# Kernel tuning notes

Hardware: AMD Instinct MI355X
Metric: run time of the kernel (lower is better)

Reference implementation:

```python
import jax, jax.numpy as jnp
import numpy as np

N, F, OUT = 8192, 256, 256


def setup_inputs() -> dict:
    key = jax.random.key(0)
    ks = jax.random.split(key, 8)
    s = 1.0 / np.sqrt(F)
    return {
        "features": jax.random.normal(ks[0], (N, F), jnp.float32),
        "key_features": jax.random.normal(ks[1], (N, F), jnp.float32),
        "adj_matrix": jax.random.uniform(ks[2], (N, N), jnp.float32),
        "W_d": jax.random.normal(ks[3], (2 * F, F), jnp.float32) * (1.0 / np.sqrt(2 * F)),
        "b_d": jnp.zeros((F,), jnp.float32),
        "W_o": jax.random.normal(ks[4], (F, OUT), jnp.float32) * s,
        "b_o": jnp.zeros((OUT,), jnp.float32),
        "W_a": jax.random.normal(ks[5], (F, F), jnp.float32) * s,
        "b_a": jnp.zeros((F,), jnp.float32),
        "W_ao": jax.random.normal(ks[6], (F, OUT), jnp.float32) * s,
        "b_ao": jnp.zeros((OUT,), jnp.float32),
    }


def reference(features, key_features, adj_matrix, W_d, b_d, W_o, b_o, W_a, b_a, W_ao, b_ao):
    n = features.shape[0]
    # masked softmax over rows; self-loop (diagonal) masked out
    neg = jnp.asarray(-1e9, adj_matrix.dtype)
    logits = adj_matrix * 5.0 + jnp.eye(n, dtype=adj_matrix.dtype) * neg
    a = jax.nn.softmax(logits, axis=-1)  # [N, N]
    # sum_j a_ij * concat(x_i, x_j) == concat(x_i * rowsum_i, (A @ X)_i)
    rowsum = jnp.sum(a, axis=-1, keepdims=True)  # == 1, kept for faithfulness
    agg = a @ features  # [N, F]
    neigh = jnp.concatenate([features * rowsum, agg], axis=-1)  # [N, 2F]
    neigh_distill = neigh @ W_d + b_d
    feature_updated = jnp.tanh((features - neigh_distill) @ W_o + b_o)
    # aggregate branch (withAgg=True)
    key_agg = (a @ key_features) @ W_a + b_a
    feature_aggregate = jnp.tanh((key_features + key_agg) @ W_ao + b_ao)
    return (feature_updated, feature_aggregate)
```

## Files before the change

kernel.cpp:

```cpp
#include <hip/hip_runtime.h>
#include <stdint.h>
#include <math.h>


typedef __attribute__((ext_vector_type(4)))  short bf16x4_t;
typedef __attribute__((ext_vector_type(8)))  short bf16x8_t;
typedef __attribute__((ext_vector_type(4)))  float f32x4_t;
typedef __attribute__((ext_vector_type(16))) float f32x16_t;

#define MFMA32(A, B, C) __builtin_amdgcn_mfma_f32_32x32x16_bf16(A, B, C, 0, 0, 0)
#define MFMA16(A, B, C) __builtin_amdgcn_mfma_f32_16x16x32_bf16(A, B, C, 0, 0, 0)

__device__ __forceinline__ unsigned short f2bf(float x) {
    union { float f; unsigned u; } c; c.f = x;
    unsigned u = c.u;
    return (unsigned short)((u + 0x7fffu + ((u >> 16) & 1u)) >> 16);
}
__device__ __forceinline__ unsigned pack2bf(float a, float b) {
    return (unsigned)f2bf(a) | ((unsigned)f2bf(b) << 16);
}
__device__ __forceinline__ float bflo(unsigned u) {
    union { unsigned u; float f; } c; c.u = u << 16; return c.f;
}
__device__ __forceinline__ float bfhi(unsigned u) {
    union { unsigned u; float f; } c; c.u = u & 0xffff0000u; return c.f;
}

__global__ __launch_bounds__(256) void transpose_f32_bf16(
    const float* __restrict__ src, unsigned short* __restrict__ dst, int R, int C)
{
    __shared__ float tile[32][33];
    const int x  = threadIdx.x & 31;
    const int y4 = (threadIdx.x >> 5) * 4;
    const int r0 = blockIdx.x * 32;
    const int c0 = blockIdx.y * 32;
#pragma unroll
    for (int i = 0; i < 4; ++i)
        tile[y4 + i][x] = src[(size_t)(r0 + y4 + i) * C + c0 + x];
    __syncthreads();
#pragma unroll
    for (int i = 0; i < 4; ++i)
        dst[(size_t)(c0 + y4 + i) * R + r0 + x] = f2bf(tile[x][y4 + i]);
}

__global__ __launch_bounds__(256) void pack_half(
    const float* __restrict__ src, unsigned* __restrict__ dst)
{
    const int idx = blockIdx.x * 256 + threadIdx.x;
    const int row = idx >> 7, cp = idx & 127;
    float2 v = *(const float2*)(src + (size_t)row * 256 + cp * 2);
    dst[(size_t)row * 256 + cp] = pack2bf(v.x, v.y);
}

__global__ __launch_bounds__(256) void compose1(
    const float* __restrict__ W_d, const float* __restrict__ W_o,
    unsigned short* __restrict__ W1t)
{
    __shared__ float wrow[256];
    const int k = blockIdx.x, t = threadIdx.x;
    wrow[t] = W_d[(size_t)k * 256 + t];
    __syncthreads();
    float acc = 0.f;
#pragma unroll 8
    for (int m = 0; m < 256; ++m) acc = fmaf(wrow[m], W_o[(size_t)m * 256 + t], acc);
    const float v = (k < 256 ? W_o[(size_t)k * 256 + t] : 0.f) - acc;
    W1t[(size_t)t * 512 + k] = f2bf(v);
}

__global__ __launch_bounds__(256) void compose2(
    const float* __restrict__ W_a, const float* __restrict__ W_ao,
    unsigned short* __restrict__ W2t)
{
    __shared__ float wrow[256];
    const int k = blockIdx.x, t = threadIdx.x;
    float v;
    if (k < 256) {
        v = W_ao[(size_t)k * 256 + t];
    } else {
        wrow[t] = W_a[(size_t)(k - 256) * 256 + t];
        __syncthreads();
        float acc = 0.f;
#pragma unroll 8
        for (int m = 0; m < 256; ++m) acc = fmaf(wrow[m], W_ao[(size_t)m * 256 + t], acc);
        v = acc;
    }
    W2t[(size_t)t * 512 + k] = f2bf(v);
}

__global__ __launch_bounds__(256) void biasC(
    const float* __restrict__ b_d, const float* __restrict__ b_o,
    const float* __restrict__ b_a, const float* __restrict__ b_ao,
    const float* __restrict__ W_o, const float* __restrict__ W_ao,
    float* __restrict__ c1, float* __restrict__ c2)
{
    const int t = threadIdx.x;
    float a1 = 0.f, a2 = 0.f;
#pragma unroll 8
    for (int m = 0; m < 256; ++m) {
        a1 = fmaf(b_d[m], W_o [(size_t)m * 256 + t], a1);
        a2 = fmaf(b_a[m], W_ao[(size_t)m * 256 + t], a2);
    }
    c1[t] = b_o[t] - a1;
    c2[t] = b_ao[t] + a2;
}

#define ROWS 128
#define KSLICE 2048
#define NIT 64
#define NCH 16
#define ASTRIDE 36

__global__ __launch_bounds__(1024) void exp_gemm(
    const float* __restrict__ adj, const unsigned short* __restrict__ Xt,
    unsigned short* __restrict__ Upart, float* __restrict__ sSp)
{
    __shared__ unsigned short sA[2][4][ROWS * ASTRIDE];

    const int t = threadIdx.x;
    const int w = t >> 6, lane = t & 63, q = lane >> 5, l31 = lane & 31;
    const int rb = blockIdx.x >> 2, h = blockIdx.x & 3;
    const int row0 = rb * ROWS, kbase = h * KSLICE;

    const int srow = t >> 3, skoff = (t & 7) * 4;
    const int sgrow = row0 + srow;
    const float* adj_row = adj + (size_t)sgrow * 8192 + kbase + skoff;
    const int swoff = srow * ASTRIDE + skoff;

    const unsigned short* bptr = Xt + (size_t)(w * 32 + l31) * 8192 + kbase + q * 8;

    float rs = 0.f;
    f32x16_t acc[4];
#pragma unroll
    for (int mt = 0; mt < 4; ++mt)
#pragma unroll
        for (int e = 0; e < 16; ++e) acc[mt][e] = 0.f;

    bf16x8_t bq[4][2];
    float4 qaA[4], qaB[4];

    auto stageChunk = [&](int cidx, const float4 (&qa)[4], int buf) {
        unsigned short* sb = &sA[buf][0][0] + swoff;
#pragma unroll
        for (int ks = 0; ks < 4; ++ks) {
            const float4 v = qa[ks];
            float e0 = __expf(5.f * v.x);
            float e1 = __expf(5.f * v.y);
            float e2 = __expf(5.f * v.z);
            float e3 = __expf(5.f * v.w);
            const int gk = kbase + (cidx * 4 + ks) * 32 + skoff;
            if (gk + 0 == sgrow) e0 = 0.f;
            if (gk + 1 == sgrow) e1 = 0.f;
            if (gk + 2 == sgrow) e2 = 0.f;
            if (gk + 3 == sgrow) e3 = 0.f;
            rs += (e0 + e1) + (e2 + e3);
            uint2 p; p.x = pack2bf(e0, e1); p.y = pack2bf(e2, e3);
            *(uint2*)(sb + ks * (ROWS * ASTRIDE)) = p;
        }
    };

    auto phase = [&](int c, float4 (&qaPre)[4], const float4 (&qaStg)[4], int buf) {
        if (c + 2 < NCH) {
#pragma unroll
            for (int ks = 0; ks < 4; ++ks)
                qaPre[ks] = *(const float4*)(adj_row + (size_t)((c + 2) * 4 + ks) * 32);
        }
        if (c + 1 < NCH) stageChunk(c + 1, qaStg, buf ^ 1);
#pragma unroll
        for (int u = 0; u < 4; ++u) {
            const int j = c * 4 + u;
            int jn = j + 2; if (jn >= NIT) jn = 0;
            bq[(u + 2) & 3][0] = *(const bf16x8_t*)(bptr + (size_t)jn * 32);
            bq[(u + 2) & 3][1] = *(const bf16x8_t*)(bptr + (size_t)jn * 32 + 16);
            const unsigned short* sa = &sA[buf][u][0] + l31 * ASTRIDE + q * 8;
#pragma unroll
            for (int s = 0; s < 2; ++s)
#pragma unroll
                for (int mt = 0; mt < 4; ++mt) {
                    const unsigned short* p = sa + mt * (32 * ASTRIDE) + s * 16;
                    bf16x4_t lo = *(const bf16x4_t*)p;
                    bf16x4_t hi = *(const bf16x4_t*)(p + 4);
                    bf16x8_t a = __builtin_shufflevector(lo, hi, 0, 1, 2, 3, 4, 5, 6, 7);
                    acc[mt] = MFMA32(a, bq[u][s], acc[mt]);
                }
        }
        asm volatile("s_waitcnt lgkmcnt(0)\n\ts_barrier" ::: "memory");
    };

#pragma unroll
    for (int ks = 0; ks < 4; ++ks)
        qaA[ks] = *(const float4*)(adj_row + (size_t)ks * 32);
#pragma unroll
    for (int ks = 0; ks < 4; ++ks)
        qaB[ks] = *(const float4*)(adj_row + (size_t)(4 + ks) * 32);
    stageChunk(0, qaA, 0);
    bq[0][0] = *(const bf16x8_t*)(bptr + 0);
    bq[0][1] = *(const bf16x8_t*)(bptr + 16);
    bq[1][0] = *(const bf16x8_t*)(bptr + 32);
    bq[1][1] = *(const bf16x8_t*)(bptr + 48);
    asm volatile("s_waitcnt lgkmcnt(0)\n\ts_barrier" ::: "memory");

    for (int c0 = 0; c0 < NCH; c0 += 2) {
        phase(c0,     qaA, qaB, 0);
        phase(c0 + 1, qaB, qaA, 1);
    }

    rs += __shfl_xor(rs, 1);
    rs += __shfl_xor(rs, 2);
    rs += __shfl_xor(rs, 4);
    if ((t & 7) == 0) sSp[h * 8192 + sgrow] = rs;

    unsigned short* up = Upart + (size_t)h * (8192 * 512) + (size_t)row0 * 512 + (w * 32 + l31);
#pragma unroll
    for (int mt = 0; mt < 4; ++mt)
#pragma unroll
        for (int reg = 0; reg < 16; ++reg) {
            const int lrow = mt * 32 + (reg & 3) + 8 * (reg >> 2) + 4 * q;
            up[(size_t)lrow * 512] = f2bf(acc[mt][reg]);
        }
}

__global__ __launch_bounds__(256) void finalize_agg(
    const unsigned* __restrict__ Upart, const float* __restrict__ sSp,
    unsigned* __restrict__ XcatN, unsigned* __restrict__ Kcat)
{
    const int row = blockIdx.x, t = threadIdx.x;
    const float inv = 1.f / (sSp[row] + sSp[8192 + row] + sSp[16384 + row] + sSp[24576 + row]);
    const unsigned* u = Upart + (size_t)row * 256 + t;
    float lo = 0.f, hi = 0.f;
#pragma unroll
    for (int hh = 0; hh < 4; ++hh) {
        const unsigned v = u[(size_t)hh * (8192 * 256)];
        lo += bflo(v); hi += bfhi(v);
    }
    const unsigned res = pack2bf(lo * inv, hi * inv);
    if (t < 128) XcatN[(size_t)row * 256 + 128 + t] = res;
    else         Kcat [(size_t)row * 256 + t];
    if (t >= 128) Kcat[(size_t)row * 256 + t] = res;
}

__global__ __launch_bounds__(256) void gemm_out(
    const unsigned short* __restrict__ A, const unsigned short* __restrict__ Wt,
    const float* __restrict__ cvec, float* __restrict__ out)
{
    __shared__ unsigned short sAm[32 * ASTRIDE];
    __shared__ unsigned short sB[256 * ASTRIDE];
    __shared__ float sBias[256];

    const int t = threadIdx.x, w = t >> 6, lane = t & 63;
    const int m_lo = lane & 15, quad = lane >> 4;
    const int row0 = blockIdx.x * 32;
    sBias[t] = cvec[t];

    f32x4_t acc[2][4];
#pragma unroll
    for (int a = 0; a < 2; ++a)
#pragma unroll
        for (int b = 0; b < 4; ++b)
#pragma unroll
            for (int e = 0; e < 4; ++e) acc[a][b][e] = 0.f;

    for (int ks = 0; ks < 16; ++ks) {
        const int k0 = ks * 32;
        __syncthreads();
        if (t < 128) {
            bf16x8_t v = *(const bf16x8_t*)(A + (size_t)(row0 + (t >> 2)) * 512 + k0 + (t & 3) * 8);
            unsigned short* d = &sAm[(t >> 2) * ASTRIDE + (t & 3) * 8];
            *(bf16x4_t*)d       = __builtin_shufflevector(v, v, 0, 1, 2, 3);
            *(bf16x4_t*)(d + 4) = __builtin_shufflevector(v, v, 4, 5, 6, 7);
        }
        {
            const unsigned short* src = Wt + (size_t)t * 512 + k0;
            unsigned short* d = &sB[t * ASTRIDE];
#pragma unroll
            for (int j = 0; j < 4; ++j) {
                bf16x8_t v = *(const bf16x8_t*)(src + j * 8);
                *(bf16x4_t*)(d + j * 8)     = __builtin_shufflevector(v, v, 0, 1, 2, 3);
                *(bf16x4_t*)(d + j * 8 + 4) = __builtin_shufflevector(v, v, 4, 5, 6, 7);
            }
        }
        __syncthreads();
        bf16x8_t a0, a1;
        {
            const unsigned short* p = &sAm[m_lo * ASTRIDE + quad * 8];
            bf16x4_t lo = *(const bf16x4_t*)p, hi = *(const bf16x4_t*)(p + 4);
            a0 = __builtin_shufflevector(lo, hi, 0, 1, 2, 3, 4, 5, 6, 7);
            p += 16 * ASTRIDE;
            lo = *(const bf16x4_t*)p; hi = *(const bf16x4_t*)(p + 4);
            a1 = __builtin_shufflevector(lo, hi, 0, 1, 2, 3, 4, 5, 6, 7);
        }
#pragma unroll
        for (int nt = 0; nt < 4; ++nt) {
            const unsigned short* p = &sB[(w * 64 + nt * 16 + m_lo) * ASTRIDE + quad * 8];
            bf16x4_t lo = *(const bf16x4_t*)p, hi = *(const bf16x4_t*)(p + 4);
            bf16x8_t b = __builtin_shufflevector(lo, hi, 0, 1, 2, 3, 4, 5, 6, 7);
            acc[0][nt] = MFMA16(a0, b, acc[0][nt]);
            acc[1][nt] = MFMA16(a1, b, acc[1][nt]);
        }
    }

#pragma unroll
    for (int mt = 0; mt < 2; ++mt)
#pragma unroll
        for (int nt = 0; nt < 4; ++nt) {
            const int col = w * 64 + nt * 16 + m_lo;
#pragma unroll
            for (int r = 0; r < 4; ++r) {
                const int row = row0 + mt * 16 + quad * 4 + r;
                out[(size_t)row * 256 + col] = tanhf(acc[mt][nt][r] + sBias[col]);
            }
        }
}

extern "C" void kernel_launch(void* const* d_in, const int* in_sizes, int n_in,
                              void* d_out, int out_size, void* d_ws, size_t ws_size,
                              hipStream_t stream) {
    const float* features = (const float*)d_in[0];
    const float* key      = (const float*)d_in[1];
    const float* adj      = (const float*)d_in[2];
    const float* W_d  = (const float*)d_in[3];
    const float* b_d  = (const float*)d_in[4];
    const float* W_o  = (const float*)d_in[5];
    const float* b_o  = (const float*)d_in[6];
    const float* W_a  = (const float*)d_in[7];
    const float* b_a  = (const float*)d_in[8];
    const float* W_ao = (const float*)d_in[9];
    const float* b_ao = (const float*)d_in[10];

    float* out1 = (float*)d_out;
    float* out2 = out1 + (size_t)8192 * 256;

    char* ws = (char*)d_ws;
    unsigned short* XcatN = (unsigned short*)(ws);
    unsigned short* Kcat  = (unsigned short*)(ws +  8388608);
    unsigned short* Xt    = (unsigned short*)(ws + 16777216);
    unsigned short* Upart = (unsigned short*)(ws + 25165824);
    float*          sSp   = (float*)         (ws + 58720256);
    unsigned short* W1t   = (unsigned short*)(ws + 58851328);
    unsigned short* W2t   = (unsigned short*)(ws + 59113472);
    float*          c1    = (float*)         (ws + 59375616);
    float*          c2    = (float*)         (ws + 59376640);

    dim3 blk(256);
    transpose_f32_bf16<<<dim3(256, 8), blk, 0, stream>>>(features, Xt, 8192, 256);
    transpose_f32_bf16<<<dim3(256, 8), blk, 0, stream>>>(key, Xt + (size_t)256 * 8192, 8192, 256);
    pack_half<<<4096, blk, 0, stream>>>(features, (unsigned*)XcatN);
    pack_half<<<4096, blk, 0, stream>>>(key, (unsigned*)Kcat);
    compose1<<<512, blk, 0, stream>>>(W_d, W_o, W1t);
    compose2<<<512, blk, 0, stream>>>(W_a, W_ao, W2t);
    biasC<<<1, blk, 0, stream>>>(b_d, b_o, b_a, b_ao, W_o, W_ao, c1, c2);

    exp_gemm<<<256, dim3(1024), 0, stream>>>(adj, Xt, Upart, sSp);
    finalize_agg<<<8192, blk, 0, stream>>>((const unsigned*)Upart, sSp,
                                           (unsigned*)XcatN, (unsigned*)Kcat);

    gemm_out<<<256, blk, 0, stream>>>(XcatN, W1t, c1, out1);
    gemm_out<<<256, blk, 0, stream>>>(Kcat,  W2t, c2, out2);
}
```

Measured before the change: 590.3 us.

## Restructure exp_gemm with async global-to-LDS loads and split output columns

The exp-weighted aggregation GEMM now streams adj tiles straight into LDS with global_load_lds, using a three-slot raw buffer. A separate pass applies exp and the diagonal mask and converts to a double-buffered bf16 tile. The grid is doubled to 512 blocks of 512 threads, each covering half of the 512 output columns, which is meant to raise occupancy and overlap memory with MFMA. The cost is that each adj tile is loaded and exponentiated by two blocks, doubling that traffic and exp work unless L2 absorbs the repeat loads. A dead load in finalize_agg is also removed.

New measurement: 607.0 us. 1.03x slower.

```diff
diff --git a/kernel.cpp b/kernel.cpp
--- a/kernel.cpp
+++ b/kernel.cpp
@@ -24,6 +24,12 @@
 }
 __device__ __forceinline__ float bfhi(unsigned u) {
     union { unsigned u; float f; } c; c.u = u & 0xffff0000u; return c.f;
+}
+
+__device__ __forceinline__ void dma16(const float* g, float* lds_base) {
+    __builtin_amdgcn_global_load_lds(
+        (const __attribute__((address_space(1))) unsigned*)g,
+        (__attribute__((address_space(3))) unsigned*)lds_base, 16, 0, 0);
 }
 
 __global__ __launch_bounds__(256) void transpose_f32_bf16(
@@ -104,119 +110,127 @@
     c2[t] = b_ao[t] + a2;
 }
 
-#define ROWS 128
-#define KSLICE 2048
-#define NIT 64
-#define NCH 16
-#define ASTRIDE 36
-
-__global__ __launch_bounds__(1024) void exp_gemm(
+#define NCHV3 64
+#define SASTR 36
+
+__global__ __launch_bounds__(512, 4) void exp_gemm(
     const float* __restrict__ adj, const unsigned short* __restrict__ Xt,
     unsigned short* __restrict__ Upart, float* __restrict__ sSp)
 {
-    __shared__ unsigned short sA[2][4][ROWS * ASTRIDE];
+    __shared__ float raw[3][4096];
+    __shared__ unsigned short sAb[2][128 * SASTR];
 
     const int t = threadIdx.x;
     const int w = t >> 6, lane = t & 63, q = lane >> 5, l31 = lane & 31;
-    const int rb = blockIdx.x >> 2, h = blockIdx.x & 3;
-    const int row0 = rb * ROWS, kbase = h * KSLICE;
-
-    const int srow = t >> 3, skoff = (t & 7) * 4;
-    const int sgrow = row0 + srow;
-    const float* adj_row = adj + (size_t)sgrow * 8192 + kbase + skoff;
-    const int swoff = srow * ASTRIDE + skoff;
-
-    const unsigned short* bptr = Xt + (size_t)(w * 32 + l31) * 8192 + kbase + q * 8;
-
-    float rs = 0.f;
-    f32x16_t acc[4];
-#pragma unroll
-    for (int mt = 0; mt < 4; ++mt)
-#pragma unroll
-        for (int e = 0; e < 16; ++e) acc[mt][e] = 0.f;
-
-    bf16x8_t bq[4][2];
-    float4 qaA[4], qaB[4];
-
-    auto stageChunk = [&](int cidx, const float4 (&qa)[4], int buf) {
-        unsigned short* sb = &sA[buf][0][0] + swoff;
-#pragma unroll
-        for (int ks = 0; ks < 4; ++ks) {
-            const float4 v = qa[ks];
+    const int b = blockIdx.x;
+    const int m  = b >> 3;
+    const int nh = b & 1;
+    const int h  = (b >> 1) & 3;
+    const int row0 = m * 128, kbase = h * 2048;
+    const int m0w = (w & 1) * 64, n0w = (w >> 1) * 64;
+
+    const int srow = t >> 3, scol = (t & 7) * 4;
+    const float* g0 = adj + (size_t)(row0 + srow) * 8192 + kbase + scol;
+    const float* g1 = g0 + (size_t)64 * 8192;
+    const int ldsW = w * 256;
+
+    const unsigned short* bB =
+        Xt + (size_t)(nh * 256 + n0w + l31) * 8192 + kbase + q * 8;
+
+    float rs0 = 0.f, rs1 = 0.f;
+    f32x16_t acc[2][2];
+#pragma unroll
+    for (int a = 0; a < 2; ++a)
+#pragma unroll
+        for (int n = 0; n < 2; ++n)
+#pragma unroll
+            for (int e = 0; e < 16; ++e) acc[a][n][e] = 0.f;
+
+    bf16x8_t bq[2][2];
+
+#define DMA_CHUNK(C, SLOT) do {                                   \
+        dma16(g0 + (size_t)(C) * 32, &raw[SLOT][ldsW]);           \
+        dma16(g1 + (size_t)(C) * 32, &raw[SLOT][2048 + ldsW]);    \
+    } while (0)
+
+#define LOADB(C) do {                                                          \
+        bq[0][0] = *(const bf16x8_t*)(bB + (size_t)(C) * 32);                  \
+        bq[0][1] = *(const bf16x8_t*)(bB + (size_t)(C) * 32 + 16);             \
+        bq[1][0] = *(const bf16x8_t*)(bB + (size_t)32 * 8192 + (size_t)(C) * 32);      \
+        bq[1][1] = *(const bf16x8_t*)(bB + (size_t)32 * 8192 + (size_t)(C) * 32 + 16); \
+    } while (0)
+
+    auto convert = [&](int c, int buf) {
+        const float* rp = &raw[c % 3][0];
+        unsigned short* sp = &sAb[buf][0];
+#pragma unroll
+        for (int half = 0; half < 2; ++half) {
+            const float4 v = *(const float4*)(rp + (size_t)t * 4 + half * 2048);
             float e0 = __expf(5.f * v.x);
             float e1 = __expf(5.f * v.y);
             float e2 = __expf(5.f * v.z);
             float e3 = __expf(5.f * v.w);
-            const int gk = kbase + (cidx * 4 + ks) * 32 + skoff;
-            if (gk + 0 == sgrow) e0 = 0.f;
-            if (gk + 1 == sgrow) e1 = 0.f;
-            if (gk + 2 == sgrow) e2 = 0.f;
-            if (gk + 3 == sgrow) e3 = 0.f;
-            rs += (e0 + e1) + (e2 + e3);
+            const int gk = kbase + c * 32 + scol;
+            const int grow = row0 + srow + half * 64;
+            if (gk + 0 == grow) e0 = 0.f;
+            if (gk + 1 == grow) e1 = 0.f;
+            if (gk + 2 == grow) e2 = 0.f;
+            if (gk + 3 == grow) e3 = 0.f;
+            const float s4 = (e0 + e1) + (e2 + e3);
+            if (half == 0) rs0 += s4; else rs1 += s4;
             uint2 p; p.x = pack2bf(e0, e1); p.y = pack2bf(e2, e3);
-            *(uint2*)(sb + ks * (ROWS * ASTRIDE)) = p;
+            *(uint2*)(sp + (size_t)(srow + half * 64) * SASTR + scol) = p;
         }
     };
 
-    auto phase = [&](int c, float4 (&qaPre)[4], const float4 (&qaStg)[4], int buf) {
-        if (c + 2 < NCH) {
-#pragma unroll
-            for (int ks = 0; ks < 4; ++ks)
-                qaPre[ks] = *(const float4*)(adj_row + (size_t)((c + 2) * 4 + ks) * 32);
-        }
-        if (c + 1 < NCH) stageChunk(c + 1, qaStg, buf ^ 1);
-#pragma unroll
-        for (int u = 0; u < 4; ++u) {
-            const int j = c * 4 + u;
-            int jn = j + 2; if (jn >= NIT) jn = 0;
-            bq[(u + 2) & 3][0] = *(const bf16x8_t*)(bptr + (size_t)jn * 32);
-            bq[(u + 2) & 3][1] = *(const bf16x8_t*)(bptr + (size_t)jn * 32 + 16);
-            const unsigned short* sa = &sA[buf][u][0] + l31 * ASTRIDE + q * 8;
-#pragma unroll
-            for (int s = 0; s < 2; ++s)
-#pragma unroll
-                for (int mt = 0; mt < 4; ++mt) {
-                    const unsigned short* p = sa + mt * (32 * ASTRIDE) + s * 16;
-                    bf16x4_t lo = *(const bf16x4_t*)p;
-                    bf16x4_t hi = *(const bf16x4_t*)(p + 4);
-                    bf16x8_t a = __builtin_shufflevector(lo, hi, 0, 1, 2, 3, 4, 5, 6, 7);
-                    acc[mt] = MFMA32(a, bq[u][s], acc[mt]);
-                }
-        }
+    DMA_CHUNK(0, 0);
+    DMA_CHUNK(1, 1);
+    asm volatile("s_waitcnt vmcnt(2) lgkmcnt(0)\n\ts_barrier" ::: "memory");
+    convert(0, 0);
+    asm volatile("s_waitcnt lgkmcnt(0)\n\ts_barrier" ::: "memory");
+
+    for (int c = 0; c < NCHV3; ++c) {
+        const int buf = c & 1;
+        LOADB(c);
+        if (c + 2 < NCHV3) DMA_CHUNK(c + 2, (c + 2) % 3);
+        const unsigned short* sp = &sAb[buf][0];
+#pragma unroll
+        for (int ks = 0; ks < 2; ++ks) {
+            bf16x8_t a0 = *(const bf16x8_t*)(sp + (size_t)(m0w + l31) * SASTR + ks * 16 + q * 8);
+            bf16x8_t a1 = *(const bf16x8_t*)(sp + (size_t)(m0w + 32 + l31) * SASTR + ks * 16 + q * 8);
+            acc[0][0] = MFMA32(a0, bq[0][ks], acc[0][0]);
+            acc[1][0] = MFMA32(a1, bq[0][ks], acc[1][0]);
+            acc[0][1] = MFMA32(a0, bq[1][ks], acc[0][1]);
+            acc[1][1] = MFMA32(a1, bq[1][ks], acc[1][1]);
+        }
+        if (c + 2 < NCHV3)
+            asm volatile("s_waitcnt vmcnt(2) lgkmcnt(0)\n\ts_barrier" ::: "memory");
+        else
+            asm volatile("s_waitcnt vmcnt(0) lgkmcnt(0)\n\ts_barrier" ::: "memory");
+        if (c + 1 < NCHV3) convert(c + 1, buf ^ 1);
         asm volatile("s_waitcnt lgkmcnt(0)\n\ts_barrier" ::: "memory");
-    };
-
-#pragma unroll
-    for (int ks = 0; ks < 4; ++ks)
-        qaA[ks] = *(const float4*)(adj_row + (size_t)ks * 32);
-#pragma unroll
-    for (int ks = 0; ks < 4; ++ks)
-        qaB[ks] = *(const float4*)(adj_row + (size_t)(4 + ks) * 32);
-    stageChunk(0, qaA, 0);
-    bq[0][0] = *(const bf16x8_t*)(bptr + 0);
-    bq[0][1] = *(const bf16x8_t*)(bptr + 16);
-    bq[1][0] = *(const bf16x8_t*)(bptr + 32);
-    bq[1][1] = *(const bf16x8_t*)(bptr + 48);
-    asm volatile("s_waitcnt lgkmcnt(0)\n\ts_barrier" ::: "memory");
-
-    for (int c0 = 0; c0 < NCH; c0 += 2) {
-        phase(c0,     qaA, qaB, 0);
-        phase(c0 + 1, qaB, qaA, 1);
-    }
-
-    rs += __shfl_xor(rs, 1);
-    rs += __shfl_xor(rs, 2);
-    rs += __shfl_xor(rs, 4);
-    if ((t & 7) == 0) sSp[h * 8192 + sgrow] = rs;
-
-    unsigned short* up = Upart + (size_t)h * (8192 * 512) + (size_t)row0 * 512 + (w * 32 + l31);
-#pragma unroll
-    for (int mt = 0; mt < 4; ++mt)
-#pragma unroll
-        for (int reg = 0; reg < 16; ++reg) {
-            const int lrow = mt * 32 + (reg & 3) + 8 * (reg >> 2) + 4 * q;
-            up[(size_t)lrow * 512] = f2bf(acc[mt][reg]);
-        }
+    }
+#undef DMA_CHUNK
+#undef LOADB
+
+    rs0 += __shfl_xor(rs0, 1); rs0 += __shfl_xor(rs0, 2); rs0 += __shfl_xor(rs0, 4);
+    rs1 += __shfl_xor(rs1, 1); rs1 += __shfl_xor(rs1, 2); rs1 += __shfl_xor(rs1, 4);
+    if (((t & 7) == 0) && nh == 0) {
+        sSp[h * 8192 + row0 + srow]      = rs0;
+        sSp[h * 8192 + row0 + srow + 64] = rs1;
+    }
+
+    unsigned short* up = Upart + (size_t)h * (8192 * 512) + (size_t)row0 * 512
+                       + (nh * 256 + n0w + l31);
+#pragma unroll
+    for (int mt = 0; mt < 2; ++mt)
+#pragma unroll
+        for (int nt = 0; nt < 2; ++nt)
+#pragma unroll
+            for (int reg = 0; reg < 16; ++reg) {
+                const int lrow = m0w + mt * 32 + (reg & 3) + 8 * (reg >> 2) + 4 * q;
+                up[(size_t)lrow * 512 + nt * 32] = f2bf(acc[mt][nt][reg]);
+            }
 }
 
 __global__ __launch_bounds__(256) void finalize_agg(
@@ -234,16 +248,15 @@
     }
     const unsigned res = pack2bf(lo * inv, hi * inv);
     if (t < 128) XcatN[(size_t)row * 256 + 128 + t] = res;
-    else         Kcat [(size_t)row * 256 + t];
-    if (t >= 128) Kcat[(size_t)row * 256 + t] = res;
+    else         Kcat [(size_t)row * 256 + t]       = res;
 }
 
 __global__ __launch_bounds__(256) void gemm_out(
     const unsigned short* __restrict__ A, const unsigned short* __restrict__ Wt,
     const float* __restrict__ cvec, float* __restrict__ out)
 {
-    __shared__ unsigned short sAm[32 * ASTRIDE];
-    __shared__ unsigned short sB[256 * ASTRIDE];
+    __shared__ unsigned short sAm[32 * SASTR];
+    __shared__ unsigned short sB[256 * SASTR];
     __shared__ float sBias[256];
 
     const int t = threadIdx.x, w = t >> 6, lane = t & 63;
@@ -255,22 +268,22 @@
 #pragma unroll
     for (int a = 0; a < 2; ++a)
 #pragma unroll
-        for (int b = 0; b < 4; ++b)
-#pragma unroll
-            for (int e = 0; e < 4; ++e) acc[a][b][e] = 0.f;
+        for (int n = 0; n < 4; ++n)
+#pragma unroll
+            for (int e = 0; e < 4; ++e) acc[a][n][e] = 0.f;
 
     for (int ks = 0; ks < 16; ++ks) {
         const int k0 = ks * 32;
         __syncthreads();
         if (t < 128) {
             bf16x8_t v = *(const bf16x8_t*)(A + (size_t)(row0 + (t >> 2)) * 512 + k0 + (t & 3) * 8);
-            unsigned short* d = &sAm[(t >> 2) * ASTRIDE + (t & 3) * 8];
+            unsigned short* d = &sAm[(t >> 2) * SASTR + (t & 3) * 8];
             *(bf16x4_t*)d       = __builtin_shufflevector(v, v, 0, 1, 2, 3);
             *(bf16x4_t*)(d + 4) = __builtin_shufflevector(v, v, 4, 5, 6, 7);
         }
         {
             const unsigned short* src = Wt + (size_t)t * 512 + k0;
-            unsigned short* d = &sB[t * ASTRIDE];
+            unsigned short* d = &sB[t * SASTR];
 #pragma unroll
             for (int j = 0; j < 4; ++j) {
                 bf16x8_t v = *(const bf16x8_t*)(src + j * 8);
@@ -281,20 +294,20 @@
         __syncthreads();
         bf16x8_t a0, a1;
         {
-            const unsigned short* p = &sAm[m_lo * ASTRIDE + quad * 8];
+            const unsigned short* p = &sAm[m_lo * SASTR + quad * 8];
             bf16x4_t lo = *(const bf16x4_t*)p, hi = *(const bf16x4_t*)(p + 4);
             a0 = __builtin_shufflevector(lo, hi, 0, 1, 2, 3, 4, 5, 6, 7);
-            p += 16 * ASTRIDE;
+            p += 16 * SASTR;
             lo = *(const bf16x4_t*)p; hi = *(const bf16x4_t*)(p + 4);
             a1 = __builtin_shufflevector(lo, hi, 0, 1, 2, 3, 4, 5, 6, 7);
         }
 #pragma unroll
         for (int nt = 0; nt < 4; ++nt) {
-            const unsigned short* p = &sB[(w * 64 + nt * 16 + m_lo) * ASTRIDE + quad * 8];
+            const unsigned short* p = &sB[(w * 64 + nt * 16 + m_lo) * SASTR + quad * 8];
             bf16x4_t lo = *(const bf16x4_t*)p, hi = *(const bf16x4_t*)(p + 4);
-            bf16x8_t b = __builtin_shufflevector(lo, hi, 0, 1, 2, 3, 4, 5, 6, 7);
-            acc[0][nt] = MFMA16(a0, b, acc[0][nt]);
-            acc[1][nt] = MFMA16(a1, b, acc[1][nt]);
+            bf16x8_t bb = __builtin_shufflevector(lo, hi, 0, 1, 2, 3, 4, 5, 6, 7);
+            acc[0][nt] = MFMA16(a0, bb, acc[0][nt]);
+            acc[1][nt] = MFMA16(a1, bb, acc[1][nt]);
         }
     }
 
@@ -349,7 +362,7 @@
     compose2<<<512, blk, 0, stream>>>(W_a, W_ao, W2t);
     biasC<<<1, blk, 0, stream>>>(b_d, b_o, b_a, b_ao, W_o, W_ao, c1, c2);
 
-    exp_gemm<<<256, dim3(1024), 0, stream>>>(adj, Xt, Upart, sSp);
+    exp_gemm<<<512, dim3(512), 0, stream>>>(adj, Xt, Upart, sSp);
     finalize_agg<<<8192, blk, 0, stream>>>((const unsigned*)Upart, sSp,
                                            (unsigned*)XcatN, (unsigned*)Kcat);
 
```
